# Kernel optimization log

Measured on AMD Instinct MI355X. Metric: run time of the kernel, lower is better.

## Reference

```python
import jax, jax.numpy as jnp
import numpy as np

B, NQ, HW, D, H = 4, 100, 4096, 1024, 16
HD = D // H  # head dim = 64
EPS = 1e-5
NEG = -1e9


def layernorm(x, g, b):
    mu = jnp.mean(x, axis=-1, keepdims=True)
    var = jnp.mean(jnp.square(x - mu), axis=-1, keepdims=True)
    return (x - mu) * jax.lax.rsqrt(var + EPS) * g + b


def setup_inputs() -> dict:
    key = jax.random.key(0)
    ks = jax.random.split(key, 6)
    scale = 0.02
    return {
        "q": jax.random.normal(ks[0], (B, NQ, D), dtype=jnp.float32),
        "kv": jax.random.normal(ks[1], (B, HW, D), dtype=jnp.float32),
        "mask": jax.random.randint(ks[2], (B, NQ, HW), 0, 2, dtype=jnp.int32),
        "in_proj_w": scale * jax.random.normal(ks[3], (3 * D, D), dtype=jnp.float32),
        "in_proj_b": jnp.zeros((3 * D,), dtype=jnp.float32),
        "out_w": scale * jax.random.normal(ks[4], (D, D), dtype=jnp.float32),
        "out_b": jnp.zeros((D,), dtype=jnp.float32),
        "g_q": jnp.ones((D,), dtype=jnp.float32),
        "b_q": jnp.zeros((D,), dtype=jnp.float32),
        "g_kv": jnp.ones((D,), dtype=jnp.float32),
        "b_kv": jnp.zeros((D,), dtype=jnp.float32),
    }


def reference(q, kv, mask, in_proj_w, in_proj_b, out_w, out_b, g_q, b_q, g_kv, b_kv):
    qn = layernorm(q, g_q, b_q)      # [B,NQ,D]
    kvn = layernorm(kv, g_kv, b_kv)  # [B,HW,D]

    # nn.MultiheadAttention fused in-projection: rows [Wq; Wk; Wv]
    Wq, Wk, Wv = jnp.split(in_proj_w, 3, axis=0)
    bq, bk, bv = jnp.split(in_proj_b, 3, axis=0)
    qp = (qn @ Wq.T + bq).reshape(B, NQ, H, HD)
    kp = (kvn @ Wk.T + bk).reshape(B, HW, H, HD)
    vp = (kvn @ Wv.T + bv).reshape(B, HW, H, HD)

    scores = jnp.einsum("bqhd,bkhd->bhqk", qp, kp) / jnp.sqrt(jnp.float32(HD))

    # Per-query key mask; a query with an all-zero mask attends everywhere
    # (original code sets key_padding_mask=None when kpm.all()).
    allowed = mask.astype(bool)                                   # [B,NQ,HW]
    has_any = jnp.any(allowed, axis=-1, keepdims=True)
    eff = jnp.where(has_any, allowed, True)
    scores = jnp.where(eff[:, None, :, :], scores, NEG)

    attn = jax.nn.softmax(scores, axis=-1)                        # [B,H,NQ,HW]
    ctx = jnp.einsum("bhqk,bkhd->bqhd", attn, vp).reshape(B, NQ, D)
    return ctx @ out_w.T + out_b
```

## Files before the change

kernel.cpp:

```cpp
#include <hip/hip_runtime.h>
#include <math.h>
#include <stdint.h>

#define B_    4
#define NQ_   100
#define HW_   4096
#define D_    1024
#define H_    16
#define HD_   64
#define NCH_  8
#define KCH_  (HW_/NCH_)
#define QT_   32
#define MP_   512

typedef __attribute__((ext_vector_type(8))) short short8;
typedef __attribute__((ext_vector_type(8))) unsigned short ushort8v;
typedef __attribute__((ext_vector_type(4))) float f32x4;

__device__ __forceinline__ unsigned short f2bf(float f) {
    unsigned int u = __float_as_uint(f);
    u += 0x7fffu + ((u >> 16) & 1u);
    return (unsigned short)(u >> 16);
}
__device__ __forceinline__ float bf2f(unsigned short h) {
    return __uint_as_float(((unsigned int)h) << 16);
}

__device__ __forceinline__ void gl2lds16(const void* g, void* l) {
    typedef __attribute__((address_space(1))) unsigned int gu32;
    typedef __attribute__((address_space(3))) unsigned int lu32;
    __builtin_amdgcn_global_load_lds(
        reinterpret_cast<gu32*>(reinterpret_cast<uintptr_t>(g)),
        reinterpret_cast<lu32*>(reinterpret_cast<uintptr_t>(l)),
        16, 0, 0);
}

#define VMCNT3() asm volatile("s_waitcnt vmcnt(3)" ::: "memory")
#define VMCNT0() asm volatile("s_waitcnt vmcnt(0)" ::: "memory")
#define BARRIER() do { __builtin_amdgcn_s_barrier(); \
                       __builtin_amdgcn_sched_barrier(0); } while (0)

__global__ __launch_bounds__(256) void ln_bf16_kernel(
    const float* __restrict__ x, const float* __restrict__ g,
    const float* __restrict__ be, unsigned short* __restrict__ y, int real_rows)
{
    const int wv = threadIdx.x >> 6, lane = threadIdx.x & 63;
    const int row = blockIdx.x * 4 + wv;
    unsigned short* yr = y + (size_t)row * D_;
    if (row >= real_rows) {
        #pragma unroll
        for (int k = 0; k < 4; ++k)
            *reinterpret_cast<ushort4*>(yr + lane*4 + k*256) = make_ushort4(0,0,0,0);
        return;
    }
    const float* xr = x + (size_t)row * D_;
    float4 v[4];
    float s = 0.f, ss = 0.f;
    #pragma unroll
    for (int k = 0; k < 4; ++k) {
        v[k] = *reinterpret_cast<const float4*>(xr + lane*4 + k*256);
        s  += v[k].x + v[k].y + v[k].z + v[k].w;
        ss += v[k].x*v[k].x + v[k].y*v[k].y + v[k].z*v[k].z + v[k].w*v[k].w;
    }
    #pragma unroll
    for (int o = 1; o < 64; o <<= 1) {
        s  += __shfl_xor(s,  o);
        ss += __shfl_xor(ss, o);
    }
    const float mu = s * (1.0f / D_);
    const float rs = rsqrtf(ss * (1.0f / D_) - mu*mu + 1e-5f);
    #pragma unroll
    for (int k = 0; k < 4; ++k) {
        const float4 gg = *reinterpret_cast<const float4*>(g  + lane*4 + k*256);
        const float4 bb = *reinterpret_cast<const float4*>(be + lane*4 + k*256);
        ushort4 o;
        o.x = f2bf((v[k].x - mu) * rs * gg.x + bb.x);
        o.y = f2bf((v[k].y - mu) * rs * gg.y + bb.y);
        o.z = f2bf((v[k].z - mu) * rs * gg.z + bb.z);
        o.w = f2bf((v[k].w - mu) * rs * gg.w + bb.w);
        *reinterpret_cast<ushort4*>(yr + lane*4 + k*256) = o;
    }
}

__global__ __launch_bounds__(256) void wconv_kernel(
    const float* __restrict__ w, unsigned short* __restrict__ wb)
{
    const int i = blockIdx.x * 256 + threadIdx.x;
    const float4 v = reinterpret_cast<const float4*>(w)[i];
    ushort4 o;
    o.x = f2bf(v.x); o.y = f2bf(v.y); o.z = f2bf(v.z); o.w = f2bf(v.w);
    reinterpret_cast<ushort4*>(wb)[i] = o;
}

__global__ __launch_bounds__(256) void hilo_a_kernel(
    const float* __restrict__ x, unsigned short* __restrict__ y)
{
    const int row = blockIdx.x;
    const int tid = threadIdx.x;
    unsigned short* yr = y + (size_t)row * 3072;
    if (row >= B_*NQ_) {
        const ushort4 z = make_ushort4(0,0,0,0);
        reinterpret_cast<ushort4*>(yr)[tid]        = z;
        reinterpret_cast<ushort4*>(yr + 1024)[tid] = z;
        reinterpret_cast<ushort4*>(yr + 2048)[tid] = z;
        return;
    }
    const float4 v = reinterpret_cast<const float4*>(x + (size_t)row * D_)[tid];
    ushort4 hi, lo;
    hi.x = f2bf(v.x); hi.y = f2bf(v.y); hi.z = f2bf(v.z); hi.w = f2bf(v.w);
    lo.x = f2bf(v.x - bf2f(hi.x)); lo.y = f2bf(v.y - bf2f(hi.y));
    lo.z = f2bf(v.z - bf2f(hi.z)); lo.w = f2bf(v.w - bf2f(hi.w));
    reinterpret_cast<ushort4*>(yr)[tid]        = hi;
    reinterpret_cast<ushort4*>(yr + 1024)[tid] = lo;
    reinterpret_cast<ushort4*>(yr + 2048)[tid] = hi;
}

__global__ __launch_bounds__(256) void hilo_w_kernel(
    const float* __restrict__ w, unsigned short* __restrict__ y)
{
    const int row = blockIdx.x;
    const int tid = threadIdx.x;
    const float4 v = reinterpret_cast<const float4*>(w + (size_t)row * D_)[tid];
    ushort4 hi, lo;
    hi.x = f2bf(v.x); hi.y = f2bf(v.y); hi.z = f2bf(v.z); hi.w = f2bf(v.w);
    lo.x = f2bf(v.x - bf2f(hi.x)); lo.y = f2bf(v.y - bf2f(hi.y));
    lo.z = f2bf(v.z - bf2f(hi.z)); lo.w = f2bf(v.w - bf2f(hi.w));
    unsigned short* yr = y + (size_t)row * 3072;
    reinterpret_cast<ushort4*>(yr)[tid]        = hi;
    reinterpret_cast<ushort4*>(yr + 1024)[tid] = hi;
    reinterpret_cast<ushort4*>(yr + 2048)[tid] = lo;
}

__global__ __launch_bounds__(256) void mpack_kernel(
    const int* __restrict__ mask, unsigned int* __restrict__ mp)
{
    const int qrow = blockIdx.x;
    const int b = blockIdx.y;
    const int tid = threadIdx.x;
    unsigned int word = 0;
    if (qrow < NQ_ && tid < 128) {
        const int4* mr = reinterpret_cast<const int4*>(
            mask + ((size_t)(b*NQ_ + qrow))*HW_ + tid*32);
        #pragma unroll
        for (int j = 0; j < 8; ++j) {
            const int4 v = mr[j];
            word |= (v.x!=0 ? 1u:0u) << (4*j);
            word |= (v.y!=0 ? 1u:0u) << (4*j+1);
            word |= (v.z!=0 ? 1u:0u) << (4*j+2);
            word |= (v.w!=0 ? 1u:0u) << (4*j+3);
        }
    }
    const int wany = __any(word != 0) ? 1 : 0;
    __shared__ int red[4];
    if ((tid & 63) == 0) red[tid >> 6] = wany;
    __syncthreads();
    const int hasany = red[0] | red[1] | red[2] | red[3];
    if (tid < 128)
        mp[((size_t)(b*128 + qrow))*128 + tid] = hasany ? word : 0xFFFFFFFFu;
}

__global__ __launch_bounds__(512, 4) void gemm_kv_kernel(
    const unsigned short* __restrict__ A, const unsigned short* __restrict__ Wb,
    const float* __restrict__ bias, unsigned short* __restrict__ kp,
    unsigned short* __restrict__ vt)
{
    extern __shared__ __align__(16) unsigned short lds[];

    const int tid  = threadIdx.x;
    const int wave = tid >> 6;
    const int lane = tid & 63;
    const int lr   = lane & 15, quad = lane >> 4;
    const int wm2  = wave >> 2;
    const int wn4  = wave & 3;

    const int x  = blockIdx.x & 7;
    const int g  = blockIdx.x >> 3;
    const int bm = x*16 + (g >> 3);
    const int bn = g & 7;

    const int srow = tid >> 2;
    const int sswz = (srow & 3) ^ ((srow >> 2) & 3);
    const int scol = ((tid & 3) ^ sswz) * 8;
    const unsigned short* aSrc  = A  + (size_t)(bm*128 + srow)*D_ + scol;
    const unsigned short* bSrc0 = Wb + (size_t)(bn*256 + srow)*D_ + scol;
    const unsigned short* bSrc1 = bSrc0 + (size_t)128*D_;
    const int wdst = wave * 512;

    int aoff[4], boff[4];
    #pragma unroll
    for (int fm = 0; fm < 4; ++fm) {
        const int row = wm2*64 + fm*16 + lr;
        aoff[fm] = row*32 + (quad ^ (row & 3) ^ ((row >> 2) & 3))*8;
    }
    #pragma unroll
    for (int fn = 0; fn < 4; ++fn) {
        const int row = wn4*64 + fn*16 + lr;
        boff[fn] = 4096 + row*32 + (quad ^ (row & 3) ^ ((row >> 2) & 3))*8;
    }

    f32x4 acc[4][4];
    #pragma unroll
    for (int i = 0; i < 4; ++i)
        #pragma unroll
        for (int j = 0; j < 4; ++j)
            acc[i][j] = (f32x4){0.f, 0.f, 0.f, 0.f};

    #pragma unroll
    for (int pt = 0; pt < 2; ++pt) {
        gl2lds16(aSrc  + pt*32, lds + pt*12288 +        wdst);
        gl2lds16(bSrc0 + pt*32, lds + pt*12288 + 4096 + wdst);
        gl2lds16(bSrc1 + pt*32, lds + pt*12288 + 8192 + wdst);
    }
    aSrc += 64; bSrc0 += 64; bSrc1 += 64;
    VMCNT3();
    BARRIER();

    int cur = 0, nx2 = 2;
    #pragma unroll 1
    for (int t = 0; t < 32; ++t) {
        const unsigned short* Sl = lds + cur*12288;
        unsigned short*       S2 = lds + nx2*12288;
        short8 afr[4], bfr[4];

        #pragma unroll
        for (int fm = 0; fm < 4; ++fm)
            afr[fm] = *reinterpret_cast<const short8*>(&Sl[aoff[fm]]);
        bfr[0] = *reinterpret_cast<const short8*>(&Sl[boff[0]]);
        bfr[1] = *reinterpret_cast<const short8*>(&Sl[boff[1]]);
        if (t < 30) {
            gl2lds16(aSrc,  S2 +        wdst);
            gl2lds16(bSrc0, S2 + 4096 + wdst);
        }
        __builtin_amdgcn_s_setprio(1);
        #pragma unroll
        for (int fm = 0; fm < 4; ++fm)
            #pragma unroll
            for (int fn = 0; fn < 2; ++fn)
                acc[fm][fn] = __builtin_amdgcn_mfma_f32_16x16x32_bf16(
                    afr[fm], bfr[fn], acc[fm][fn], 0, 0, 0);
        __builtin_amdgcn_s_setprio(0);

        bfr[2] = *reinterpret_cast<const short8*>(&Sl[boff[2]]);
        bfr[3] = *reinterpret_cast<const short8*>(&Sl[boff[3]]);
        if (t < 30) {
            gl2lds16(bSrc1, S2 + 8192 + wdst);
            aSrc += 32; bSrc0 += 32; bSrc1 += 32;
        }
        __builtin_amdgcn_s_setprio(1);
        #pragma unroll
        for (int fm = 0; fm < 4; ++fm)
            #pragma unroll
            for (int fn = 2; fn < 4; ++fn)
                acc[fm][fn] = __builtin_amdgcn_mfma_f32_16x16x32_bf16(
                    afr[fm], bfr[fn], acc[fm][fn], 0, 0, 0);
        __builtin_amdgcn_s_setprio(0);

        if (t < 30)       { VMCNT3(); }
        else if (t == 30) { VMCNT0(); }
        BARRIER();
        cur = (cur == 2) ? 0 : cur + 1;
        nx2 = (nx2 == 2) ? 0 : nx2 + 1;
    }

    const int colbase = bn*256 + wn4*64 + lr;
    const int mbase   = bm*128 + wm2*64 + quad*4;
    if (bn < 4) {
        #pragma unroll
        for (int fn = 0; fn < 4; ++fn) {
            const int n = colbase + fn*16;
            const float bb = bias[n];
            #pragma unroll
            for (int fm = 0; fm < 4; ++fm) {
                unsigned short* Cp = kp + (size_t)(mbase + fm*16)*1024 + n;
                #pragma unroll
                for (int r = 0; r < 4; ++r)
                    Cp[(size_t)r * 1024] = f2bf(acc[fm][fn][r] + bb);
            }
        }
    } else {
        const int b = bm >> 5;
        const int key0 = mbase - b*4096;
        #pragma unroll
        for (int fn = 0; fn < 4; ++fn) {
            const int n = colbase + fn*16;
            const float bb = bias[n];
            unsigned short* vrow = vt + (size_t)(b*1024 + n - 1024) * HW_;
            #pragma unroll
            for (int fm = 0; fm < 4; ++fm) {
                ushort4 o;
                o.x = f2bf(acc[fm][fn][0] + bb);
                o.y = f2bf(acc[fm][fn][1] + bb);
                o.z = f2bf(acc[fm][fn][2] + bb);
                o.w = f2bf(acc[fm][fn][3] + bb);
                *reinterpret_cast<ushort4*>(vrow + key0 + fm*16) = o;
            }
        }
    }
}

__global__ __launch_bounds__(256) void gemm_splitk_kernel(
    const unsigned short* __restrict__ A, const unsigned short* __restrict__ W,
    float* __restrict__ P, int K, int KS)
{
    __shared__ __align__(16) unsigned short As[2048];
    __shared__ __align__(16) unsigned short Bs[2048];
    const int tid = threadIdx.x;
    const int wave = tid >> 6, lane = tid & 63;
    const int lr = lane & 15, quad = lane >> 4;
    const int bn = blockIdx.x, bm = blockIdx.y, sk = blockIdx.z;

    const int r0 = tid >> 2;
    const int xs = (r0 & 3) ^ ((r0 >> 2) & 3);
    const int kc = (tid & 3) ^ xs;
    const unsigned short* ap = A + (size_t)(bm*64 + r0)*K + sk*KS + kc*8;
    const unsigned short* bp = W + (size_t)(bn*64 + r0)*K + sk*KS + kc*8;
    unsigned short* asd = As + wave*512;
    unsigned short* bsd = Bs + wave*512;

    f32x4 acc[4];
    #pragma unroll
    for (int j = 0; j < 4; ++j) acc[j] = (f32x4){0.f,0.f,0.f,0.f};

    const int arow = wave*16 + lr;
    const int xa = (arow & 3) ^ ((arow >> 2) & 3);
    const int aoff = (arow*4 + (quad ^ xa))*8;
    int boff[4];
    #pragma unroll
    for (int j = 0; j < 4; ++j) {
        const int brow = j*16 + lr;
        const int xb = (brow & 3) ^ ((brow >> 2) & 3);
        boff[j] = (brow*4 + (quad ^ xb))*8;
    }

    const int nsteps = KS >> 5;
    for (int s = 0; s < nsteps; ++s) {
        gl2lds16(ap, asd); gl2lds16(bp, bsd);
        ap += 32; bp += 32;
        __syncthreads();
        const short8 af = *reinterpret_cast<const short8*>(&As[aoff]);
        short8 bf[4];
        #pragma unroll
        for (int j = 0; j < 4; ++j)
            bf[j] = *reinterpret_cast<const short8*>(&Bs[boff[j]]);
        #pragma unroll
        for (int j = 0; j < 4; ++j)
            acc[j] = __builtin_amdgcn_mfma_f32_16x16x32_bf16(af, bf[j], acc[j], 0, 0, 0);
        __syncthreads();
    }

    float* Pb = P + ((size_t)sk*MP_ + bm*64)*1024 + bn*64;
    const int m0 = wave*16 + quad*4;
    #pragma unroll
    for (int j = 0; j < 4; ++j)
        #pragma unroll
        for (int r = 0; r < 4; ++r)
            Pb[(size_t)(m0 + r)*1024 + j*16 + lr] = acc[j][r];
}

__global__ __launch_bounds__(256) void reduce_kernel(
    const float* __restrict__ P, const float* __restrict__ bias,
    float* __restrict__ Cout, int SK)
{
    const int i4 = blockIdx.x * 256 + threadIdx.x;
    const int c4 = i4 & 255;
    float4 s = reinterpret_cast<const float4*>(bias)[c4];
    for (int sk = 0; sk < SK; ++sk) {
        const float4 p = reinterpret_cast<const float4*>(P + (size_t)sk*MP_*1024)[i4];
        s.x += p.x; s.y += p.y; s.z += p.z; s.w += p.w;
    }
    reinterpret_cast<float4*>(Cout)[i4] = s;
}

__global__ __launch_bounds__(256) void flash_kernel(
    const float* __restrict__ qp, const unsigned short* __restrict__ kp,
    const unsigned short* __restrict__ vt, const unsigned int* __restrict__ mpack,
    float* __restrict__ partO, float* __restrict__ partL)
{
    __shared__ __align__(16) unsigned char smem[49152];
    unsigned short* Ks  = (unsigned short*)smem;
    unsigned short* Vts = (unsigned short*)(smem + 16384);
    unsigned short* Qs  = (unsigned short*)(smem + 32768);
    unsigned short* Ps  = (unsigned short*)(smem + 37376);
    unsigned int*   MWs = (unsigned int*)  (smem + 47616);
    float*          mlW = (float*)         (smem + 48128);
    float*          Om  = (float*)smem;

    const int tid = threadIdx.x;
    const int wave = tid >> 6, lane = tid & 63;
    const int lr = lane & 15, quad = lane >> 4;
    const int qt = blockIdx.x, h = blockIdx.y;
    const int b = blockIdx.z >> 3, ks = blockIdx.z & 7;
    const int kb0 = ks * KCH_;

    {
        const int q = tid >> 3, dc = (tid & 7) * 8;
        const int qg = qt*QT_ + q;
        float4 v0 = make_float4(0.f,0.f,0.f,0.f), v1 = v0;
        if (qg < NQ_) {
            const float* src = qp + ((size_t)(b*NQ_ + qg))*D_ + h*HD_ + dc;
            v0 = *reinterpret_cast<const float4*>(src);
            v1 = *reinterpret_cast<const float4*>(src + 4);
        }
        ushort8v o;
        o[0]=f2bf(v0.x*0.125f); o[1]=f2bf(v0.y*0.125f);
        o[2]=f2bf(v0.z*0.125f); o[3]=f2bf(v0.w*0.125f);
        o[4]=f2bf(v1.x*0.125f); o[5]=f2bf(v1.y*0.125f);
        o[6]=f2bf(v1.z*0.125f); o[7]=f2bf(v1.w*0.125f);
        *reinterpret_cast<ushort8v*>(&Qs[q*72 + dc]) = o;
    }

    const unsigned short* kptr[4];
    const unsigned short* vptr[4];
    #pragma unroll
    for (int i = 0; i < 4; ++i) {
        const int s = i*256 + tid;
        const int key = s >> 3, jg = (s & 7) ^ (key & 7);
        kptr[i] = kp + ((size_t)(b*HW_) + kb0 + key)*1024 + h*HD_ + jg*8;
        const int d = s >> 4, js = s & 15, jg2 = js ^ (d & 15);
        vptr[i] = vt + ((size_t)(b*1024 + h*HD_ + d))*HW_ + kb0 + jg2*8;
    }

    int koff[2][2], voff[4];
    #pragma unroll
    for (int kj = 0; kj < 2; ++kj)
        #pragma unroll
        for (int ds = 0; ds < 2; ++ds) {
            const int key_l = wave*32 + kj*16 + lr;
            const int jg = ds*4 + quad;
            koff[kj][ds] = (key_l*8 + (jg ^ (key_l & 7))) * 8;
        }
    #pragma unroll
    for (int dj = 0; dj < 4; ++dj) {
        const int d_l = dj*16 + lr;
        const int jg = wave*4 + quad;
        voff[dj] = (d_l*16 + (jg ^ (d_l & 15))) * 8;
    }

    float lreg[8];
    #pragma unroll
    for (int i = 0; i < 8; ++i) lreg[i] = 0.f;
    f32x4 Ov[2][4];
    #pragma unroll
    for (int i = 0; i < 2; ++i)
        #pragma unroll
        for (int j = 0; j < 4; ++j)
            Ov[i][j] = (f32x4){0.f,0.f,0.f,0.f};

    for (int kt = 0; kt < 4; ++kt) {
        __syncthreads();
        #pragma unroll
        for (int i = 0; i < 4; ++i) {
            gl2lds16(kptr[i], Ks  + (i*256 + wave*64)*8);
            gl2lds16(vptr[i], Vts + (i*256 + wave*64)*8);
            kptr[i] += 128*1024; vptr[i] += 128;
        }
        if (tid < 128) {
            const int mw = tid >> 5, mq = tid & 31;
            MWs[mw*32 + mq] = mpack[((size_t)(b*128 + qt*QT_ + mq))*128 +
                                    (ks*16 + kt*4 + mw)];
        }
        __syncthreads();

        f32x4 S[2][2];
        #pragma unroll
        for (int i = 0; i < 2; ++i)
            #pragma unroll
            for (int kj = 0; kj < 2; ++kj)
                S[i][kj] = (f32x4){0.f,0.f,0.f,0.f};
        #pragma unroll
        for (int ds = 0; ds < 2; ++ds) {
            short8 aq[2], bk[2];
            aq[0] = *reinterpret_cast<const short8*>(&Qs[(     lr)*72 + ds*32 + quad*8]);
            aq[1] = *reinterpret_cast<const short8*>(&Qs[(16 + lr)*72 + ds*32 + quad*8]);
            bk[0] = *reinterpret_cast<const short8*>(&Ks[koff[0][ds]]);
            bk[1] = *reinterpret_cast<const short8*>(&Ks[koff[1][ds]]);
            #pragma unroll
            for (int i = 0; i < 2; ++i)
                #pragma unroll
                for (int kj = 0; kj < 2; ++kj)
                    S[i][kj] = __builtin_amdgcn_mfma_f32_16x16x32_bf16(
                        aq[i], bk[kj], S[i][kj], 0, 0, 0);
        }

        #pragma unroll
        for (int i = 0; i < 2; ++i) {
            #pragma unroll
            for (int r = 0; r < 4; ++r) {
                const int q = i*16 + quad*4 + r;
                const unsigned int mw = MWs[wave*32 + q];
                const float p0 = ((mw >> lr) & 1u)        ? __expf(S[i][0][r]) : 0.f;
                const float p1 = ((mw >> (16 + lr)) & 1u) ? __expf(S[i][1][r]) : 0.f;
                lreg[i*4+r] += p0 + p1;
                const float p0n = __shfl_xor(p0, 1);
                const float p1n = __shfl_xor(p1, 1);
                if (!(lr & 1)) {
                    const unsigned int w0 = (unsigned)f2bf(p0) | ((unsigned)f2bf(p0n) << 16);
                    const unsigned int w1 = (unsigned)f2bf(p1) | ((unsigned)f2bf(p1n) << 16);
                    *reinterpret_cast<unsigned int*>(&Ps[wave*1280 + q*40 + lr])      = w0;
                    *reinterpret_cast<unsigned int*>(&Ps[wave*1280 + q*40 + 16 + lr]) = w1;
                }
            }
        }

        short8 pf[2], vf[4];
        #pragma unroll
        for (int i = 0; i < 2; ++i)
            pf[i] = *reinterpret_cast<const short8*>(&Ps[wave*1280 + (i*16+lr)*40 + quad*8]);
        #pragma unroll
        for (int dj = 0; dj < 4; ++dj)
            vf[dj] = *reinterpret_cast<const short8*>(&Vts[voff[dj]]);
        #pragma unroll
        for (int i = 0; i < 2; ++i)
            #pragma unroll
            for (int dj = 0; dj < 4; ++dj)
                Ov[i][dj] = __builtin_amdgcn_mfma_f32_16x16x32_bf16(
                    pf[i], vf[dj], Ov[i][dj], 0, 0, 0);
    }

    __syncthreads();
    #pragma unroll
    for (int i = 0; i < 2; ++i)
        #pragma unroll
        for (int r = 0; r < 4; ++r) {
            float l = lreg[i*4+r];
            #pragma unroll
            for (int o = 1; o < 16; o <<= 1) l += __shfl_xor(l, o);
            if (lr == 0) mlW[wave*32 + i*16 + quad*4 + r] = l;
        }
    #pragma unroll
    for (int i = 0; i < 2; ++i)
        #pragma unroll
        for (int dj = 0; dj < 4; ++dj)
            #pragma unroll
            for (int r = 0; r < 4; ++r) {
                const int q = i*16 + quad*4 + r;
                Om[wave*2112 + q*66 + dj*16 + lr] = Ov[i][dj][r];
            }
    __syncthreads();
    {
        const int q = tid >> 3, dc = (tid & 7) * 8;
        float L = 0.f;
        #pragma unroll
        for (int w = 0; w < 4; ++w) L += mlW[w*32 + q];
        float os[8] = {};
        #pragma unroll
        for (int w = 0; w < 4; ++w)
            #pragma unroll
            for (int j = 0; j < 8; ++j)
                os[j] += Om[w*2112 + q*66 + dc + j];
        const size_t pr = (((size_t)(b*H_ + h))*NCH_ + ks)*128 + qt*QT_ + q;
        *reinterpret_cast<float4*>(&partO[pr*HD_ + dc])     = make_float4(os[0],os[1],os[2],os[3]);
        *reinterpret_cast<float4*>(&partO[pr*HD_ + dc + 4]) = make_float4(os[4],os[5],os[6],os[7]);
        if ((tid & 7) == 0) partL[pr] = L;
    }
}

__global__ __launch_bounds__(64) void combine_kernel(
    const float* __restrict__ partO, const float* __restrict__ partL,
    float* __restrict__ ctx)
{
    const int d = threadIdx.x;
    const int qi = blockIdx.x, h = blockIdx.y, b = blockIdx.z;
    const size_t base = ((size_t)(b*H_ + h)) * NCH_ * 128;
    float L = 0.f, O = 0.f;
    #pragma unroll
    for (int i = 0; i < NCH_; ++i) {
        const size_t r = base + i*128 + qi;
        L += partL[r];
        O += partO[r*HD_ + d];
    }
    ctx[((size_t)(b*NQ_ + qi))*D_ + h*HD_ + d] = O / L;
}

extern "C" void kernel_launch(void* const* d_in, const int* in_sizes, int n_in,
                              void* d_out, int out_size, void* d_ws, size_t ws_size,
                              hipStream_t stream)
{
    const float* q     = (const float*)d_in[0];
    const float* kv    = (const float*)d_in[1];
    const int*   mask  = (const int*)  d_in[2];
    const float* in_w  = (const float*)d_in[3];
    const float* in_b  = (const float*)d_in[4];
    const float* out_w = (const float*)d_in[5];
    const float* out_b = (const float*)d_in[6];
    const float* g_q   = (const float*)d_in[7];
    const float* b_q   = (const float*)d_in[8];
    const float* g_kv  = (const float*)d_in[9];
    const float* b_kv  = (const float*)d_in[10];
    float* out = (float*)d_out;

    char* ws = (char*)d_ws;
    float*          qp       = (float*)         (ws + 0);
    unsigned int*   mpackp   = (unsigned int*)  (ws + 1638400);
    unsigned short* wfull_bf = (unsigned short*)(ws + 1900544);
    unsigned short* qn_bf    = (unsigned short*)(ws + 8192000);
    unsigned short* ctx_cat  = (unsigned short*)(ws + 9240576);
    unsigned short* wout_cat = (unsigned short*)(ws + 12386304);
    float*          P        = (float*)         (ws + 18677760);
    float*          ctx      = (float*)         (ws + 35454976);
    float*          partL    = (float*)         (ws + 37093376);
    float*          partO    = (float*)         (ws + 37355520);
    unsigned short* kvn_bf   = (unsigned short*)(ws + 54132736);
    unsigned short* kp       = (unsigned short*)(ws + 87687168);
    unsigned short* vt       = (unsigned short*)(ws + 121241600);

    static bool attr_set = false;
    if (!attr_set) {
        hipFuncSetAttribute(reinterpret_cast<const void*>(gemm_kv_kernel),
                            hipFuncAttributeMaxDynamicSharedMemorySize, 73728);
        attr_set = true;
    }

    mpack_kernel<<<dim3(128, B_), 256, 0, stream>>>(mask, mpackp);
    wconv_kernel<<<3*D_*D_/4/256, 256, 0, stream>>>(in_w, wfull_bf);
    ln_bf16_kernel<<<B_*HW_/4, 256, 0, stream>>>(kv, g_kv, b_kv, kvn_bf, B_*HW_);
    ln_bf16_kernel<<<MP_/4, 256, 0, stream>>>(q, g_q, b_q, qn_bf, B_*NQ_);

    gemm_splitk_kernel<<<dim3(D_/64, MP_/64, 8), 256, 0, stream>>>(
        qn_bf, wfull_bf, P, D_, 128);
    reduce_kernel<<<B_*NQ_*D_/4/256, 256, 0, stream>>>(P, in_b, qp, 8);

    gemm_kv_kernel<<<dim3(1024), 512, 73728, stream>>>(
        kvn_bf, wfull_bf + (size_t)D_*D_, in_b + D_, kp, vt);

    flash_kernel<<<dim3(4, H_, B_*NCH_), 256, 0, stream>>>(
        qp, kp, vt, mpackp, partO, partL);
    combine_kernel<<<dim3(NQ_, H_, B_), 64, 0, stream>>>(partO, partL, ctx);

    hilo_a_kernel<<<MP_, 256, 0, stream>>>(ctx, ctx_cat);
    hilo_w_kernel<<<D_, 256, 0, stream>>>(out_w, wout_cat);
    gemm_splitk_kernel<<<dim3(D_/64, MP_/64, 8), 256, 0, stream>>>(
        ctx_cat, wout_cat, P, 3*D_, 384);
    reduce_kernel<<<B_*NQ_*D_/4/256, 256, 0, stream>>>(P, out_b, out, 8);
}
```

Measured before the change: 313.3 us.

## Shrink KV GEMM tile to 128x128 with 4 waves and halve flash key splits

The KV projection GEMM moves from 512-thread blocks with 128x256 tiles to 256-thread blocks with 128x128 tiles, doubling the grid and cutting LDS per block from 72KB to 48KB so more blocks fit per CU. The loaders are reorganised to issue four 16-byte global-to-LDS copies per stage, with the wait count adjusted to match. Separately, the flash attention kernel splits the keys into 4 chunks instead of 8, so each block loops over more key tiles and there are fewer partial results to combine. The smaller GEMM tile lowers operand reuse per block, and fewer flash chunks cut the grid size and so parallelism.

Result: no change. 314.8 us (+0.5%).

```diff
diff --git a/kernel.cpp b/kernel.cpp
--- a/kernel.cpp
+++ b/kernel.cpp
@@ -8,7 +8,7 @@
 #define D_    1024
 #define H_    16
 #define HD_   64
-#define NCH_  8
+#define NCH_  4
 #define KCH_  (HW_/NCH_)
 #define QT_   32
 #define MP_   512
@@ -35,7 +35,7 @@
         16, 0, 0);
 }
 
-#define VMCNT3() asm volatile("s_waitcnt vmcnt(3)" ::: "memory")
+#define VMCNT4() asm volatile("s_waitcnt vmcnt(4)" ::: "memory")
 #define VMCNT0() asm volatile("s_waitcnt vmcnt(0)" ::: "memory")
 #define BARRIER() do { __builtin_amdgcn_s_barrier(); \
                        __builtin_amdgcn_sched_barrier(0); } while (0)
@@ -159,7 +159,7 @@
         mp[((size_t)(b*128 + qrow))*128 + tid] = hasany ? word : 0xFFFFFFFFu;
 }
 
-__global__ __launch_bounds__(512, 4) void gemm_kv_kernel(
+__global__ __launch_bounds__(256, 3) void gemm_kv_kernel(
     const unsigned short* __restrict__ A, const unsigned short* __restrict__ Wb,
     const float* __restrict__ bias, unsigned short* __restrict__ kp,
     unsigned short* __restrict__ vt)
@@ -170,31 +170,32 @@
     const int wave = tid >> 6;
     const int lane = tid & 63;
     const int lr   = lane & 15, quad = lane >> 4;
-    const int wm2  = wave >> 2;
-    const int wn4  = wave & 3;
+    const int wm   = wave >> 1;
+    const int wn   = wave & 1;
 
     const int x  = blockIdx.x & 7;
     const int g  = blockIdx.x >> 3;
-    const int bm = x*16 + (g >> 3);
-    const int bn = g & 7;
+    const int bm = x*16 + (g >> 4);
+    const int bn = g & 15;
 
     const int srow = tid >> 2;
     const int sswz = (srow & 3) ^ ((srow >> 2) & 3);
     const int scol = ((tid & 3) ^ sswz) * 8;
-    const unsigned short* aSrc  = A  + (size_t)(bm*128 + srow)*D_ + scol;
-    const unsigned short* bSrc0 = Wb + (size_t)(bn*256 + srow)*D_ + scol;
-    const unsigned short* bSrc1 = bSrc0 + (size_t)128*D_;
+    const unsigned short* aSrc0 = A  + (size_t)(bm*128 + srow     )*D_ + scol;
+    const unsigned short* aSrc1 = A  + (size_t)(bm*128 + srow + 64)*D_ + scol;
+    const unsigned short* bSrc0 = Wb + (size_t)(bn*128 + srow     )*D_ + scol;
+    const unsigned short* bSrc1 = Wb + (size_t)(bn*128 + srow + 64)*D_ + scol;
     const int wdst = wave * 512;
 
     int aoff[4], boff[4];
     #pragma unroll
     for (int fm = 0; fm < 4; ++fm) {
-        const int row = wm2*64 + fm*16 + lr;
+        const int row = wm*64 + fm*16 + lr;
         aoff[fm] = row*32 + (quad ^ (row & 3) ^ ((row >> 2) & 3))*8;
     }
     #pragma unroll
     for (int fn = 0; fn < 4; ++fn) {
-        const int row = wn4*64 + fn*16 + lr;
+        const int row = wn*64 + fn*16 + lr;
         boff[fn] = 4096 + row*32 + (quad ^ (row & 3) ^ ((row >> 2) & 3))*8;
     }
 
@@ -207,19 +208,20 @@
 
     #pragma unroll
     for (int pt = 0; pt < 2; ++pt) {
-        gl2lds16(aSrc  + pt*32, lds + pt*12288 +        wdst);
-        gl2lds16(bSrc0 + pt*32, lds + pt*12288 + 4096 + wdst);
-        gl2lds16(bSrc1 + pt*32, lds + pt*12288 + 8192 + wdst);
-    }
-    aSrc += 64; bSrc0 += 64; bSrc1 += 64;
-    VMCNT3();
+        gl2lds16(aSrc0 + pt*32, lds + pt*8192 +        wdst);
+        gl2lds16(aSrc1 + pt*32, lds + pt*8192 + 2048 + wdst);
+        gl2lds16(bSrc0 + pt*32, lds + pt*8192 + 4096 + wdst);
+        gl2lds16(bSrc1 + pt*32, lds + pt*8192 + 6144 + wdst);
+    }
+    aSrc0 += 64; aSrc1 += 64; bSrc0 += 64; bSrc1 += 64;
+    VMCNT4();
     BARRIER();
 
     int cur = 0, nx2 = 2;
     #pragma unroll 1
     for (int t = 0; t < 32; ++t) {
-        const unsigned short* Sl = lds + cur*12288;
-        unsigned short*       S2 = lds + nx2*12288;
+        const unsigned short* Sl = lds + cur*8192;
+        unsigned short*       S2 = lds + nx2*8192;
         short8 afr[4], bfr[4];
 
         #pragma unroll
@@ -228,8 +230,8 @@
         bfr[0] = *reinterpret_cast<const short8*>(&Sl[boff[0]]);
         bfr[1] = *reinterpret_cast<const short8*>(&Sl[boff[1]]);
         if (t < 30) {
-            gl2lds16(aSrc,  S2 +        wdst);
-            gl2lds16(bSrc0, S2 + 4096 + wdst);
+            gl2lds16(aSrc0, S2 +        wdst);
+            gl2lds16(aSrc1, S2 + 2048 + wdst);
         }
         __builtin_amdgcn_s_setprio(1);
         #pragma unroll
@@ -243,8 +245,9 @@
         bfr[2] = *reinterpret_cast<const short8*>(&Sl[boff[2]]);
         bfr[3] = *reinterpret_cast<const short8*>(&Sl[boff[3]]);
         if (t < 30) {
-            gl2lds16(bSrc1, S2 + 8192 + wdst);
-            aSrc += 32; bSrc0 += 32; bSrc1 += 32;
+            gl2lds16(bSrc0, S2 + 4096 + wdst);
+            gl2lds16(bSrc1, S2 + 6144 + wdst);
+            aSrc0 += 32; aSrc1 += 32; bSrc0 += 32; bSrc1 += 32;
         }
         __builtin_amdgcn_s_setprio(1);
         #pragma unroll
@@ -255,16 +258,16 @@
                     afr[fm], bfr[fn], acc[fm][fn], 0, 0, 0);
         __builtin_amdgcn_s_setprio(0);
 
-        if (t < 30)       { VMCNT3(); }
+        if (t < 30)       { VMCNT4(); }
         else if (t == 30) { VMCNT0(); }
         BARRIER();
         cur = (cur == 2) ? 0 : cur + 1;
         nx2 = (nx2 == 2) ? 0 : nx2 + 1;
     }
 
-    const int colbase = bn*256 + wn4*64 + lr;
-    const int mbase   = bm*128 + wm2*64 + quad*4;
-    if (bn < 4) {
+    const int colbase = bn*128 + wn*64 + lr;
+    const int mbase   = bm*128 + wm*64 + quad*4;
+    if (bn < 8) {
         #pragma unroll
         for (int fn = 0; fn < 4; ++fn) {
             const int n = colbase + fn*16;
@@ -389,7 +392,7 @@
     const int wave = tid >> 6, lane = tid & 63;
     const int lr = lane & 15, quad = lane >> 4;
     const int qt = blockIdx.x, h = blockIdx.y;
-    const int b = blockIdx.z >> 3, ks = blockIdx.z & 7;
+    const int b = blockIdx.z / NCH_, ks = blockIdx.z % NCH_;
     const int kb0 = ks * KCH_;
 
     {
@@ -446,7 +449,7 @@
         for (int j = 0; j < 4; ++j)
             Ov[i][j] = (f32x4){0.f,0.f,0.f,0.f};
 
-    for (int kt = 0; kt < 4; ++kt) {
+    for (int kt = 0; kt < KCH_/128; ++kt) {
         __syncthreads();
         #pragma unroll
         for (int i = 0; i < 4; ++i) {
@@ -457,7 +460,7 @@
         if (tid < 128) {
             const int mw = tid >> 5, mq = tid & 31;
             MWs[mw*32 + mq] = mpack[((size_t)(b*128 + qt*QT_ + mq))*128 +
-                                    (ks*16 + kt*4 + mw)];
+                                    (ks*(KCH_/32) + kt*4 + mw)];
         }
         __syncthreads();
 
@@ -607,7 +610,7 @@
     static bool attr_set = false;
     if (!attr_set) {
         hipFuncSetAttribute(reinterpret_cast<const void*>(gemm_kv_kernel),
-                            hipFuncAttributeMaxDynamicSharedMemorySize, 73728);
+                            hipFuncAttributeMaxDynamicSharedMemorySize, 49152);
         attr_set = true;
     }
 
@@ -620,7 +623,7 @@
         qn_bf, wfull_bf, P, D_, 128);
     reduce_kernel<<<B_*NQ_*D_/4/256, 256, 0, stream>>>(P, in_b, qp, 8);
 
-    gemm_kv_kernel<<<dim3(1024), 512, 73728, stream>>>(
+    gemm_kv_kernel<<<dim3(2048), 256, 49152, stream>>>(
         kvn_bf, wfull_bf + (size_t)D_*D_, in_b + D_, kp, vt);
 
     flash_kernel<<<dim3(4, H_, B_*NCH_), 256, 0, stream>>>(
```

## Double-buffer K/V tiles in flash kernel and halve key splits

Applied to the files above, without the earlier changes.

Flash attention now double-buffers its K/V and mask tiles in LDS. The next tile's asynchronous global-to-LDS load is issued right after the barrier, so memory latency overlaps the MFMA and softmax work on the current tile. The key dimension is split into 4 chunks instead of 8, so each block runs twice as many iterations and fewer partial results are left for combine. LDS use rises to about 80KB of dynamic shared memory per block, which lowers occupancy and halves the number of blocks launched. That could offset the gain from hiding latency.

Result: no change. 311.2 us (-0.7%).

```diff
diff --git a/kernel.cpp b/kernel.cpp
--- a/kernel.cpp
+++ b/kernel.cpp
@@ -8,8 +8,9 @@
 #define D_    1024
 #define H_    16
 #define HD_   64
-#define NCH_  8
+#define NCH_  4
 #define KCH_  (HW_/NCH_)
+#define NT_   (KCH_/128)
 #define QT_   32
 #define MP_   512
 
@@ -37,6 +38,7 @@
 
 #define VMCNT3() asm volatile("s_waitcnt vmcnt(3)" ::: "memory")
 #define VMCNT0() asm volatile("s_waitcnt vmcnt(0)" ::: "memory")
+#define VMLG0()  asm volatile("s_waitcnt vmcnt(0) lgkmcnt(0)" ::: "memory")
 #define BARRIER() do { __builtin_amdgcn_s_barrier(); \
                        __builtin_amdgcn_sched_barrier(0); } while (0)
 
@@ -376,20 +378,20 @@
     const unsigned short* __restrict__ vt, const unsigned int* __restrict__ mpack,
     float* __restrict__ partO, float* __restrict__ partL)
 {
-    __shared__ __align__(16) unsigned char smem[49152];
+    extern __shared__ __align__(16) unsigned char smem[];
     unsigned short* Ks  = (unsigned short*)smem;
-    unsigned short* Vts = (unsigned short*)(smem + 16384);
-    unsigned short* Qs  = (unsigned short*)(smem + 32768);
-    unsigned short* Ps  = (unsigned short*)(smem + 37376);
-    unsigned int*   MWs = (unsigned int*)  (smem + 47616);
-    float*          mlW = (float*)         (smem + 48128);
+    unsigned short* Vts = (unsigned short*)(smem + 32768);
+    unsigned short* Qs  = (unsigned short*)(smem + 65536);
+    unsigned short* Ps  = (unsigned short*)(smem + 70144);
+    unsigned int*   MWs = (unsigned int*)  (smem + 80384);
+    float*          mlW = (float*)         (smem + 65536);
     float*          Om  = (float*)smem;
 
     const int tid = threadIdx.x;
     const int wave = tid >> 6, lane = tid & 63;
     const int lr = lane & 15, quad = lane >> 4;
     const int qt = blockIdx.x, h = blockIdx.y;
-    const int b = blockIdx.z >> 3, ks = blockIdx.z & 7;
+    const int b = blockIdx.z / NCH_, ks = blockIdx.z % NCH_;
     const int kb0 = ks * KCH_;
 
     {
@@ -446,20 +448,31 @@
         for (int j = 0; j < 4; ++j)
             Ov[i][j] = (f32x4){0.f,0.f,0.f,0.f};
 
-    for (int kt = 0; kt < 4; ++kt) {
-        __syncthreads();
-        #pragma unroll
-        for (int i = 0; i < 4; ++i) {
-            gl2lds16(kptr[i], Ks  + (i*256 + wave*64)*8);
-            gl2lds16(vptr[i], Vts + (i*256 + wave*64)*8);
-            kptr[i] += 128*1024; vptr[i] += 128;
-        }
-        if (tid < 128) {
-            const int mw = tid >> 5, mq = tid & 31;
-            MWs[mw*32 + mq] = mpack[((size_t)(b*128 + qt*QT_ + mq))*128 +
-                                    (ks*16 + kt*4 + mw)];
-        }
-        __syncthreads();
+    #define STAGE_KT(kt_)                                                     \
+        do {                                                                  \
+            const int buf_ = (kt_) & 1;                                       \
+            _Pragma("unroll")                                                 \
+            for (int i = 0; i < 4; ++i) {                                     \
+                gl2lds16(kptr[i], Ks  + buf_*8192 + (i*256 + wave*64)*8);     \
+                gl2lds16(vptr[i], Vts + buf_*8192 + (i*256 + wave*64)*8);     \
+                kptr[i] += 128*1024; vptr[i] += 128;                          \
+            }                                                                 \
+            if (tid < 128) {                                                  \
+                const int mw_ = tid >> 5, mq_ = tid & 31;                     \
+                MWs[buf_*128 + mw_*32 + mq_] =                                \
+                    mpack[((size_t)(b*128 + qt*QT_ + mq_))*128 +              \
+                          (ks*(KCH_/32) + (kt_)*4 + mw_)];                    \
+            }                                                                 \
+        } while (0)
+
+    STAGE_KT(0);
+
+    #pragma unroll 1
+    for (int kt = 0; kt < NT_; ++kt) {
+        const int buf = kt & 1;
+        VMLG0();
+        BARRIER();
+        if (kt + 1 < NT_) STAGE_KT(kt + 1);
 
         f32x4 S[2][2];
         #pragma unroll
@@ -472,8 +485,8 @@
             short8 aq[2], bk[2];
             aq[0] = *reinterpret_cast<const short8*>(&Qs[(     lr)*72 + ds*32 + quad*8]);
             aq[1] = *reinterpret_cast<const short8*>(&Qs[(16 + lr)*72 + ds*32 + quad*8]);
-            bk[0] = *reinterpret_cast<const short8*>(&Ks[koff[0][ds]]);
-            bk[1] = *reinterpret_cast<const short8*>(&Ks[koff[1][ds]]);
+            bk[0] = *reinterpret_cast<const short8*>(&Ks[buf*8192 + koff[0][ds]]);
+            bk[1] = *reinterpret_cast<const short8*>(&Ks[buf*8192 + koff[1][ds]]);
             #pragma unroll
             for (int i = 0; i < 2; ++i)
                 #pragma unroll
@@ -487,7 +500,7 @@
             #pragma unroll
             for (int r = 0; r < 4; ++r) {
                 const int q = i*16 + quad*4 + r;
-                const unsigned int mw = MWs[wave*32 + q];
+                const unsigned int mw = MWs[buf*128 + wave*32 + q];
                 const float p0 = ((mw >> lr) & 1u)        ? __expf(S[i][0][r]) : 0.f;
                 const float p1 = ((mw >> (16 + lr)) & 1u) ? __expf(S[i][1][r]) : 0.f;
                 lreg[i*4+r] += p0 + p1;
@@ -508,7 +521,7 @@
             pf[i] = *reinterpret_cast<const short8*>(&Ps[wave*1280 + (i*16+lr)*40 + quad*8]);
         #pragma unroll
         for (int dj = 0; dj < 4; ++dj)
-            vf[dj] = *reinterpret_cast<const short8*>(&Vts[voff[dj]]);
+            vf[dj] = *reinterpret_cast<const short8*>(&Vts[buf*8192 + voff[dj]]);
         #pragma unroll
         for (int i = 0; i < 2; ++i)
             #pragma unroll
@@ -516,6 +529,7 @@
                 Ov[i][dj] = __builtin_amdgcn_mfma_f32_16x16x32_bf16(
                     pf[i], vf[dj], Ov[i][dj], 0, 0, 0);
     }
+    #undef STAGE_KT
 
     __syncthreads();
     #pragma unroll
@@ -608,6 +622,8 @@
     if (!attr_set) {
         hipFuncSetAttribute(reinterpret_cast<const void*>(gemm_kv_kernel),
                             hipFuncAttributeMaxDynamicSharedMemorySize, 73728);
+        hipFuncSetAttribute(reinterpret_cast<const void*>(flash_kernel),
+                            hipFuncAttributeMaxDynamicSharedMemorySize, 81408);
         attr_set = true;
     }
 
@@ -623,7 +639,7 @@
     gemm_kv_kernel<<<dim3(1024), 512, 73728, stream>>>(
         kvn_bf, wfull_bf + (size_t)D_*D_, in_b + D_, kp, vt);
 
-    flash_kernel<<<dim3(4, H_, B_*NCH_), 256, 0, stream>>>(
+    flash_kernel<<<dim3(4, H_, B_*NCH_), 256, 81408, stream>>>(
         qp, kp, vt, mpackp, partO, partL);
     combine_kernel<<<dim3(NQ_, H_, B_), 64, 0, stream>>>(partO, partL, ctx);
 
```
